# Optimization experiments

Measured on AMD Instinct MI355X. Metric: run time of the kernel, lower is better.

Reference implementation:

```python
import jax, jax.numpy as jnp
from jax import lax
import numpy as np

DN = ('NCWXYZ', 'OIWXYZ', 'NCWXYZ')  # 4 spatial dims W,X,Y,Z

def _conv4d(x, w, b):
    # x: [B, Cin, S, S, S, S]; w: [Cout, Cin, k, k, k, k]; valid padding, stride 1
    y = lax.conv_general_dilated(x, w, window_strides=(1, 1, 1, 1),
                                 padding='VALID', dimension_numbers=DN)
    return y + b[None, :, None, None, None, None]

def setup_inputs() -> dict:
    key = jax.random.key(0)
    ks = jax.random.split(key, 16)
    def rn(k, shape, fan_in):
        return jax.random.normal(k, shape, dtype=jnp.float32) * (2.0 / fan_in) ** 0.5
    B = 256
    x = jax.random.normal(ks[0], (B, 1, 18, 18, 18, 18), dtype=jnp.float32)
    w1 = rn(ks[1], (3, 1, 4, 4, 4, 4), 1 * 4**4); b1 = jnp.zeros((3,), jnp.float32)
    w2 = rn(ks[2], (3, 3, 4, 4, 4, 4), 3 * 4**4); b2 = jnp.zeros((3,), jnp.float32)
    w3 = rn(ks[3], (4, 3, 4, 4, 4, 4), 3 * 4**4); b3 = jnp.zeros((4,), jnp.float32)
    w4 = rn(ks[4], (5, 4, 4, 4, 4, 4), 4 * 4**4); b4 = jnp.zeros((5,), jnp.float32)
    w5 = rn(ks[5], (5, 5, 3, 3, 3, 3), 5 * 3**4); b5 = jnp.zeros((5,), jnp.float32)
    dw1 = rn(ks[6], (33, 1280), 1280); db1 = jnp.zeros((33,), jnp.float32)
    dw2 = rn(ks[7], (2, 33), 33); db2 = jnp.zeros((2,), jnp.float32)
    return {'x': x, 'w1': w1, 'b1': b1, 'w2': w2, 'b2': b2, 'w3': w3, 'b3': b3,
            'w4': w4, 'b4': b4, 'w5': w5, 'b5': b5,
            'dw1': dw1, 'db1': db1, 'dw2': dw2, 'db2': db2}

def reference(x, w1, b1, w2, b2, w3, b3, w4, b4, w5, b5, dw1, db1, dw2, db2):
    h = jax.nn.relu(_conv4d(x, w1, b1))   # [B,3,15,15,15,15]
    h = jax.nn.relu(_conv4d(h, w2, b2))   # [B,3,12,12,12,12]
    h = jax.nn.relu(_conv4d(h, w3, b3))   # [B,4,9,9,9,9]
    h = jax.nn.relu(_conv4d(h, w4, b4))   # [B,5,6,6,6,6]
    h = jax.nn.relu(_conv4d(h, w5, b5))   # [B,5,4,4,4,4]
    h = h.reshape(h.shape[0], -1)         # [B,1280]
    # Dropout treated as identity (eval-mode reference)
    h = jax.nn.relu(h @ dw1.T + db1)      # [B,33]
    return jax.nn.softmax(h @ dw2.T + db2, axis=1)  # [B,2]
```

## Files before the change

kernel.cpp:

```cpp
#include <hip/hip_runtime.h>
#include <hip/hip_bf16.h>
#include <math.h>


#define BATCH 256
typedef _Float16 half_t;
typedef _Float16 h2_t  __attribute__((ext_vector_type(2)));
typedef short    bf16x8 __attribute__((ext_vector_type(8)));
typedef float    f32x4 __attribute__((ext_vector_type(4)));
typedef unsigned int   uint32;
typedef unsigned short ushort16;

__device__ __forceinline__ float dot2f(uint32 a, uint32 b, float c) {
    return __builtin_amdgcn_fdot2(__builtin_bit_cast(h2_t, a),
                                  __builtin_bit_cast(h2_t, b), c, false);
}

__device__ __forceinline__ ushort16 f2bf(float f) {
    const uint32 u = __builtin_bit_cast(uint32, f);
    return (ushort16)((u + 0x7FFFu + ((u >> 16) & 1u)) >> 16);
}

__global__ void cvt_x_pad(const float* __restrict__ x,
                          ushort16* __restrict__ xp) {
    constexpr int CH  = 972;
    constexpr int NSL = BATCH * 18;
    const int c = blockIdx.x * blockDim.x + threadIdx.x;
    if (c >= NSL * CH) return;
    const int s   = c / CH;
    const int j   = c - s * CH;
    const int r   = j / 3;
    const int g   = j - 3 * r;
    const float* src = x + ((size_t)s * 324 + r) * 18 + 8 * g;
    uint32 w[4];
    if (g < 2) {
        #pragma unroll
        for (int q = 0; q < 4; ++q) {
            const float2 v = ((const float2*)src)[q];
            w[q] = (uint32)f2bf(v.x) | ((uint32)f2bf(v.y) << 16);
        }
    } else {
        const float2 v = *(const float2*)src;
        w[0] = (uint32)f2bf(v.x) | ((uint32)f2bf(v.y) << 16);
        w[1] = w[2] = w[3] = 0;
    }
    ((uint4*)xp)[c] = (uint4){w[0], w[1], w[2], w[3]};
}

template <int CIN, int COUT, int ISZ, int OSZ, int ZPK, int KS>
__device__ void pack_mfma_one(const float* __restrict__ w,
                              ushort16* __restrict__ Bq, int gtid, int gstride) {
    constexpr int TOT = 4 * KS * COUT * 512;
    for (int t = gtid; t < TOT; t += gstride) {
        const int h  = t & 7;
        const int l  = (t >> 3) & 63;
        const int f  = t >> 9;
        const int nt = f % COUT;
        const int ks = (f / COUT) % KS;
        const int kw = f / (COUT * KS);
        const int k  = ks * 32 + (l >> 4) * 8 + h;
        const int combo = k / ZPK;
        const int iz = k - combo * ZPK;
        const int ci = combo >> 4;
        const int kx = (combo >> 2) & 3;
        const int ky = combo & 3;
        const int oz = l & 15;
        const int kz = iz - oz;
        ushort16 v = 0;
        if (oz < OSZ && kz >= 0 && kz < 4 && iz < ISZ)
            v = f2bf(w[((((nt * CIN + ci) * 4 + kw) * 4 + kx) * 4 + ky) * 4 + kz]);
        Bq[t] = v;
    }
}

__global__ void pack_weights_mfma(const float* __restrict__ w1,
                                  const float* __restrict__ w2,
                                  const float* __restrict__ w3,
                                  ushort16* __restrict__ Bq1,
                                  ushort16* __restrict__ Bq2,
                                  ushort16* __restrict__ Bq3) {
    const int gtid = blockIdx.x * blockDim.x + threadIdx.x;
    const int gs   = gridDim.x * blockDim.x;
    pack_mfma_one<1, 3, 18, 15, 24, 12>(w1, Bq1, gtid, gs);
    pack_mfma_one<3, 3, 15, 12, 16, 24>(w2, Bq2, gtid, gs);
    pack_mfma_one<3, 4, 12,  9, 16, 24>(w3, Bq3, gtid, gs);
}

template <int CIN, int COUT, int ISZ, int OSZ, int ZPK, int KS,
          int MT_TOT, int NT, int IN_MODE, bool OUTF16>
__global__ __launch_bounds__(NT)
void conv4d_mfma(const void* __restrict__ in_v,
                 const ushort16* __restrict__ Bq,
                 const float* __restrict__ bias,
                 ushort16* __restrict__ out) {
    constexpr int K   = 4;
    constexpr int R2  = ISZ * ISZ;
    constexpr int NW  = NT / 64;
    constexpr int MT_PER = (MT_TOT + NW - 1) / NW;
    constexpr int SLAB = (CIN * R2 + 24) * ZPK;
    static_assert(CIN * 16 * ZPK == KS * 32, "K-dim bookkeeping");
    static_assert(ZPK % 8 == 0, "8-slice must not straddle combos");

    __shared__ ushort16 slab[SLAB];

    const int tid = threadIdx.x;
    const int l   = tid & 63;
    const int wv  = tid >> 6;
    const int b   = blockIdx.x / OSZ;
    const int ow  = blockIdx.x % OSZ;
    const int lg  = l >> 4;

    for (int t = tid; t < SLAB; t += NT) slab[t] = 0;

    int mbase[MT_PER];
    #pragma unroll
    for (int i = 0; i < MT_PER; ++i) {
        const int mt = wv + NW * i;
        const int m  = (mt < MT_TOT) ? (mt * 16 + (l & 15)) : 0;
        mbase[i] = (m / OSZ) * ISZ + (m % OSZ);
    }

    f32x4 acc[MT_PER][COUT];
    #pragma unroll
    for (int i = 0; i < MT_PER; ++i)
        #pragma unroll
        for (int nt = 0; nt < COUT; ++nt)
            acc[i][nt] = (f32x4){0.f, 0.f, 0.f, 0.f};

    for (int kw = 0; kw < K; ++kw) {
        __syncthreads();
        const int iw = ow + kw;
        if constexpr (IN_MODE == 0) {
            const float* g = (const float*)in_v +
                ((size_t)b * ISZ + iw) * (size_t)(R2 * ISZ);
            for (int t = tid; t < (R2 * ISZ) / 2; t += NT) {
                const float2 v = ((const float2*)g)[t];
                const int e = 2 * t;
                const int r = e / ISZ, z = e % ISZ;
                const uint32 pv = (uint32)f2bf(v.x) | ((uint32)f2bf(v.y) << 16);
                *(uint32*)&slab[r * ZPK + z] = pv;
            }
        } else {
            constexpr int CPR = ZPK / 8;
            constexpr int NCH = CIN * R2 * CPR;
            const ushort16* inp = (const ushort16*)in_v;
            for (int t = tid; t < NCH; t += NT) {
                const int ci  = t / (R2 * CPR);
                const int rem = t % (R2 * CPR);
                const uint4* g = (const uint4*)(inp +
                    ((size_t)(b * CIN + ci) * ISZ + iw) * (size_t)(R2 * ZPK));
                const uint4 v = g[rem];
                *(uint4*)&slab[(ci * R2) * ZPK + rem * 8] = v;
            }
        }
        __syncthreads();

        #pragma unroll 2
        for (int ks = 0; ks < KS; ++ks) {
            bf16x8 bq[COUT];
            const ushort16* bp = Bq + (size_t)((kw * KS + ks) * COUT) * 512 + l * 8;
            #pragma unroll
            for (int nt = 0; nt < COUT; ++nt)
                bq[nt] = *(const bf16x8*)(bp + nt * 512);
            const int k8    = ks * 32 + lg * 8;
            const int combo = k8 / ZPK;
            const int iz0   = k8 - combo * ZPK;
            const int ci    = combo >> 4;
            const int kx    = (combo >> 2) & 3;
            const int ky    = combo & 3;
            const int roff  = ci * R2 + kx * ISZ + ky;
            #pragma unroll
            for (int i = 0; i < MT_PER; ++i) {
                if (wv + NW * i < MT_TOT) {
                    const bf16x8 a =
                        *(const bf16x8*)&slab[(mbase[i] + roff) * ZPK + iz0];
                    #pragma unroll
                    for (int nt = 0; nt < COUT; ++nt)
                        acc[i][nt] = __builtin_amdgcn_mfma_f32_16x16x32_bf16(
                            a, bq[nt], acc[i][nt], 0, 0, 0);
                }
            }
        }
    }

    const int oz = l & 15;
    #pragma unroll
    for (int i = 0; i < MT_PER; ++i) {
        const int mt = wv + NW * i;
        if (mt < MT_TOT) {
            #pragma unroll
            for (int nt = 0; nt < COUT; ++nt) {
                const float bv = bias[nt];
                #pragma unroll
                for (int r = 0; r < 4; ++r) {
                    const int m = mt * 16 + (l >> 4) * 4 + r;
                    if (m < OSZ * OSZ) {
                        const int ox = m / OSZ, oy = m % OSZ;
                        const float vv = fmaxf(acc[i][nt][r] + bv, 0.f);
                        ushort16 bits;
                        if constexpr (OUTF16) {
                            const half_t hv = (half_t)vv;
                            bits = __builtin_bit_cast(ushort16, hv);
                        } else {
                            bits = f2bf(vv);
                        }
                        out[(((((size_t)b * COUT + nt) * OSZ + ow) * OSZ + ox)
                             * OSZ + oy) * 16 + oz] = bits;
                    }
                }
            }
        }
    }
}

template <int CIN, int COUT, int K, int ISZ, int OSZ,
          int IPG, int OPG, int ZP, int NT, bool INF32>
__global__ __launch_bounds__(NT)
void conv4d_relu_f16(const void* __restrict__ in_v,
                     const float* __restrict__ w,
                     const float* __restrict__ bias,
                     half_t* __restrict__ out) {
    constexpr int KP  = 4;
    constexpr int R2  = ISZ * ISZ;
    constexpr int WTOT = CIN * K * K * K * COUT * KP;
    constexpr int LINES = COUT * OSZ * OSZ;
    constexpr int NIT = (LINES + NT - 1) / NT;
    constexpr int RL  = OSZ + KP - 1;
    constexpr int RQ  = (RL + 7) / 8;
    constexpr int NW  = RQ * 4;
    constexpr int NODD = (OSZ + 2) / 2;

    static_assert(8 * RQ <= ZP, "row read overruns z-pad");
    static_assert(NODD + 1 <= NW, "perm source word out of range");

    __shared__ half_t sw[WTOT];
    __shared__ half_t slab[CIN * R2 * ZP];

    const int tid = threadIdx.x;
    const int b   = blockIdx.x / OSZ;
    const int ow  = blockIdx.x % OSZ;

    for (int t = tid; t < WTOT; t += NT) {
        const int kz = t % KP; int c = t / KP;
        const int co = c % COUT; c /= COUT;
        const int ky = c % K; c /= K;
        const int kx = c % K; c /= K;
        const int kw = c % K; const int ci = c / K;
        const float v = (kz < K)
            ? w[((((co * CIN + ci) * K + kw) * K + kx) * K + ky) * K + kz]
            : 0.0f;
        sw[t] = (half_t)v;
    }

    float acc[NIT][OSZ];
    #pragma unroll
    for (int it = 0; it < NIT; ++it) {
        const int line = tid + it * NT;
        const float bv = (line < LINES) ? bias[line % COUT] : 0.0f;
        #pragma unroll
        for (int oz = 0; oz < OSZ; ++oz) acc[it][oz] = bv;
    }

    for (int kw = 0; kw < K; ++kw) {
        __syncthreads();
        const int iw = ow + kw;
        if constexpr (INF32) {
            const float* g = (const float*)in_v + ((size_t)b * ISZ + iw) * (size_t)(R2 * ISZ);
            for (int t = tid; t < R2 * ISZ; t += NT) {
                const int r = t / ISZ, z = t % ISZ;
                slab[r * ZP + z] = (half_t)g[t];
            }
        } else {
            constexpr int CPR = IPG / 8;
            constexpr int NCH = CIN * R2 * CPR;
            const half_t* inp = (const half_t*)in_v;
            for (int t = tid; t < NCH; t += NT) {
                const int ci  = t / (R2 * CPR);
                const int rem = t % (R2 * CPR);
                const int r = rem / CPR, c = rem % CPR;
                const uint4* g = (const uint4*)(inp +
                    ((size_t)(b * CIN + ci) * ISZ + iw) * (size_t)(R2 * IPG));
                const uint4 v = g[rem];
                *(uint4*)&slab[(ci * R2 + r) * ZP + 8 * c] = v;
            }
        }
        __syncthreads();

        #pragma unroll
        for (int it = 0; it < NIT; ++it) {
            const int line = tid + it * NT;
            if (line >= LINES) continue;
            const int co = line % COUT;
            const int xy = line / COUT;
            const int ox = xy / OSZ;
            const int oy = xy % OSZ;
            #pragma unroll 1
            for (int ci = 0; ci < CIN; ++ci) {
                #pragma unroll 1
                for (int kx = 0; kx < K; ++kx) {
                    #pragma unroll
                    for (int ky = 0; ky < K; ++ky) {
                        const half_t* rp = &slab[((ci * ISZ + ox + kx) * ISZ + oy + ky) * ZP];
                        uint32 wd[NW];
                        #pragma unroll
                        for (int q = 0; q < RQ; ++q) {
                            const uint4 v = ((const uint4*)rp)[q];
                            wd[4*q+0] = v.x; wd[4*q+1] = v.y;
                            wd[4*q+2] = v.z; wd[4*q+3] = v.w;
                        }
                        uint32 od[NODD];
                        #pragma unroll
                        for (int i = 0; i < NODD; ++i)
                            od[i] = __builtin_amdgcn_perm(wd[i + 1], wd[i], 0x05040302u);
                        const int wb = ((((ci * K + kw) * K + kx) * K + ky) * COUT + co) * KP;
                        const uint2 wv = *(const uint2*)&sw[wb];
                        #pragma unroll
                        for (int oz = 0; oz < OSZ; ++oz) {
                            const int s1 = oz + 2;
                            const uint32 p0 = (oz & 1) ? od[oz >> 1] : wd[oz >> 1];
                            const uint32 p1 = (s1 & 1) ? od[s1 >> 1] : wd[s1 >> 1];
                            acc[it][oz] = dot2f(p0, wv.x, dot2f(p1, wv.y, acc[it][oz]));
                        }
                    }
                }
            }
        }
    }

    #pragma unroll
    for (int it = 0; it < NIT; ++it) {
        const int line = tid + it * NT;
        if (line >= LINES) continue;
        const int co = line % COUT;
        const int xy = line / COUT;
        const int ox = xy / OSZ;
        const int oy = xy % OSZ;
        half_t* op = out + (((((size_t)b * COUT + co) * OSZ + ow) * OSZ + ox) * OSZ + oy) * OPG;
        #pragma unroll
        for (int p = 0; p < OSZ / 2; ++p) {
            h2_t pv = { (half_t)fmaxf(acc[it][2*p],     0.0f),
                        (half_t)fmaxf(acc[it][2*p + 1], 0.0f) };
            ((uint32*)op)[p] = __builtin_bit_cast(uint32, pv);
        }
        if constexpr (OSZ & 1)
            op[OSZ - 1] = (half_t)fmaxf(acc[it][OSZ - 1], 0.0f);
    }
}

__global__ void dense1_relu_f16(const half_t* __restrict__ h,
                                const float* __restrict__ w,
                                const float* __restrict__ bias,
                                float* __restrict__ out) {
    int idx = blockIdx.x * blockDim.x + threadIdx.x;
    if (idx >= BATCH * 33) return;
    const int j = idx % 33;
    const int i = idx / 33;
    const half_t* hr = h + (size_t)i * 1280;
    const float*  wr = w + (size_t)j * 1280;
    float a0 = bias[j], a1 = 0.f, a2 = 0.f, a3 = 0.f;
    for (int k = 0; k < 1280; k += 4) {
        a0 = fmaf((float)hr[k + 0], wr[k + 0], a0);
        a1 = fmaf((float)hr[k + 1], wr[k + 1], a1);
        a2 = fmaf((float)hr[k + 2], wr[k + 2], a2);
        a3 = fmaf((float)hr[k + 3], wr[k + 3], a3);
    }
    out[idx] = fmaxf((a0 + a1) + (a2 + a3), 0.0f);
}

__global__ void dense2_softmax(const float* __restrict__ h,
                               const float* __restrict__ w,
                               const float* __restrict__ bias,
                               float* __restrict__ out) {
    int i = blockIdx.x * blockDim.x + threadIdx.x;
    if (i >= BATCH) return;
    const float* hr = h + (size_t)i * 33;
    float a0 = bias[0], a1 = bias[1];
    for (int k = 0; k < 33; ++k) {
        a0 = fmaf(hr[k], w[k], a0);
        a1 = fmaf(hr[k], w[33 + k], a1);
    }
    const float m = fmaxf(a0, a1);
    const float e0 = expf(a0 - m);
    const float e1 = expf(a1 - m);
    const float s = e0 + e1;
    out[i * 2 + 0] = e0 / s;
    out[i * 2 + 1] = e1 / s;
}

extern "C" void kernel_launch(void* const* d_in, const int* in_sizes, int n_in,
                              void* d_out, int out_size, void* d_ws, size_t ws_size,
                              hipStream_t stream) {
    const float* x   = (const float*)d_in[0];
    const float* w1  = (const float*)d_in[1];
    const float* b1  = (const float*)d_in[2];
    const float* w2  = (const float*)d_in[3];
    const float* b2  = (const float*)d_in[4];
    const float* w3  = (const float*)d_in[5];
    const float* b3  = (const float*)d_in[6];
    const float* w4  = (const float*)d_in[7];
    const float* b4  = (const float*)d_in[8];
    const float* w5  = (const float*)d_in[9];
    const float* b5  = (const float*)d_in[10];
    const float* dw1 = (const float*)d_in[11];
    const float* db1 = (const float*)d_in[12];
    const float* dw2 = (const float*)d_in[13];
    const float* db2 = (const float*)d_in[14];

    ushort16* wsA = (ushort16*)d_ws;
    ushort16* wsB = wsA + 42000000;

    ushort16* h1 = wsA;
    ushort16* xp = wsB;
    ushort16* h2 = wsB;
    ushort16* h3 = wsA;
    half_t*   h4 = (half_t*)wsB;
    half_t*   h5 = (half_t*)wsA;
    float*    h6 = (float*)(wsB + 8000000);
    ushort16* Bq1 = wsA + 41500000;
    ushort16* Bq2 = wsA + 41600000;
    ushort16* Bq3 = wsA + 41760000;
    float* outp = (float*)d_out;

    const bool big_ws = ws_size >= (size_t)155663616ull;

    hipLaunchKernelGGL(pack_weights_mfma, dim3(64), dim3(256), 0, stream,
                       w1, w2, w3, Bq1, Bq2, Bq3);

    if (big_ws) {
        constexpr int NCH = BATCH * 18 * 972;
        hipLaunchKernelGGL(cvt_x_pad, dim3((NCH + 255) / 256), dim3(256),
                           0, stream, x, xp);
        hipLaunchKernelGGL((conv4d_mfma<1, 3, 18, 15, 24, 12, 15, 256, 2, false>),
                           dim3(BATCH * 15), dim3(256), 0, stream, xp, Bq1, b1, h1);
    } else {
        hipLaunchKernelGGL((conv4d_mfma<1, 3, 18, 15, 24, 12, 15, 256, 0, false>),
                           dim3(BATCH * 15), dim3(256), 0, stream, x, Bq1, b1, h1);
    }
    hipLaunchKernelGGL((conv4d_mfma<3, 3, 15, 12, 16, 24, 9, 256, 2, false>),
                       dim3(BATCH * 12), dim3(256), 0, stream, h1, Bq2, b2, h2);
    hipLaunchKernelGGL((conv4d_mfma<3, 4, 12, 9, 16, 24, 6, 256, 2, true>),
                       dim3(BATCH * 9), dim3(256), 0, stream, h2, Bq3, b3, h3);
    hipLaunchKernelGGL((conv4d_relu_f16<4, 5, 4, 9, 6, 16, 8, 24, 192, false>),
                       dim3(BATCH * 6), dim3(192), 0, stream, h3, w4, b4, h4);
    hipLaunchKernelGGL((conv4d_relu_f16<5, 5, 3, 6, 4, 8, 4, 8, 128, false>),
                       dim3(BATCH * 4), dim3(128), 0, stream, h4, w5, b5, h5);
    {
        dim3 grid((BATCH * 33 + 255) / 256);
        hipLaunchKernelGGL(dense1_relu_f16, grid, dim3(256), 0, stream, h5, dw1, db1, h6);
    }
    {
        hipLaunchKernelGGL(dense2_softmax, dim3(1), dim3(256), 0, stream,
                           h6, dw2, db2, outp);
    }
}
```

Baseline: 759.4 us.

## Move conv layer 4 onto bf16 MFMA path and pad LDS slab stride

Layer 4 now runs on the MFMA bf16 implicit-GEMM kernel with a new weight-packing kernel, replacing the scalar f16 dot-product kernel. Layer 3 output switches from f16 to bf16 to feed it. The conv kernel gains separate LDS row stride (ZS), input z-stride (IPZ) and output z-stride (OZS) parameters, so slab rows are padded to 24 elements, likely to reduce LDS bank conflicts. Risks include precision change and the extra pack launch.

```diff
diff --git a/kernel.cpp b/kernel.cpp
--- a/kernel.cpp
+++ b/kernel.cpp
@@ -86,8 +86,15 @@
     pack_mfma_one<3, 4, 12,  9, 16, 24>(w3, Bq3, gtid, gs);
 }
 
+__global__ void pack_weights_mfma4(const float* __restrict__ w4,
+                                   ushort16* __restrict__ Bq4) {
+    const int gtid = blockIdx.x * blockDim.x + threadIdx.x;
+    const int gs   = gridDim.x * blockDim.x;
+    pack_mfma_one<4, 5, 9, 6, 16, 32>(w4, Bq4, gtid, gs);
+}
+
 template <int CIN, int COUT, int ISZ, int OSZ, int ZPK, int KS,
-          int MT_TOT, int NT, int IN_MODE, bool OUTF16>
+          int MT_TOT, int NT, int IN_MODE, bool OUTF16, int ZS, int IPZ, int OZS>
 __global__ __launch_bounds__(NT)
 void conv4d_mfma(const void* __restrict__ in_v,
                  const ushort16* __restrict__ Bq,
@@ -97,9 +104,10 @@
     constexpr int R2  = ISZ * ISZ;
     constexpr int NW  = NT / 64;
     constexpr int MT_PER = (MT_TOT + NW - 1) / NW;
-    constexpr int SLAB = (CIN * R2 + 24) * ZPK;
+    constexpr int SLAB = (CIN * R2 + 24) * ZS;
     static_assert(CIN * 16 * ZPK == KS * 32, "K-dim bookkeeping");
     static_assert(ZPK % 8 == 0, "8-slice must not straddle combos");
+    static_assert(ZS >= ZPK && IPZ >= ZPK, "strides must cover logical K rows");
 
     __shared__ ushort16 slab[SLAB];
 
@@ -138,19 +146,26 @@
                 const int e = 2 * t;
                 const int r = e / ISZ, z = e % ISZ;
                 const uint32 pv = (uint32)f2bf(v.x) | ((uint32)f2bf(v.y) << 16);
-                *(uint32*)&slab[r * ZPK + z] = pv;
+                *(uint32*)&slab[r * ZS + z] = pv;
             }
         } else {
-            constexpr int CPR = ZPK / 8;
+            constexpr int CPR = IPZ / 8;
             constexpr int NCH = CIN * R2 * CPR;
             const ushort16* inp = (const ushort16*)in_v;
             for (int t = tid; t < NCH; t += NT) {
                 const int ci  = t / (R2 * CPR);
                 const int rem = t % (R2 * CPR);
                 const uint4* g = (const uint4*)(inp +
-                    ((size_t)(b * CIN + ci) * ISZ + iw) * (size_t)(R2 * ZPK));
+                    ((size_t)(b * CIN + ci) * ISZ + iw) * (size_t)(R2 * IPZ));
                 const uint4 v = g[rem];
-                *(uint4*)&slab[(ci * R2) * ZPK + rem * 8] = v;
+                int dst;
+                if constexpr (IPZ == ZS) {
+                    dst = (ci * R2) * ZS + rem * 8;
+                } else {
+                    const int r = rem / CPR, c = rem % CPR;
+                    dst = (ci * R2 + r) * ZS + c * 8;
+                }
+                *(uint4*)&slab[dst] = v;
             }
         }
         __syncthreads();
@@ -173,7 +188,7 @@
             for (int i = 0; i < MT_PER; ++i) {
                 if (wv + NW * i < MT_TOT) {
                     const bf16x8 a =
-                        *(const bf16x8*)&slab[(mbase[i] + roff) * ZPK + iz0];
+                        *(const bf16x8*)&slab[(mbase[i] + roff) * ZS + iz0];
                     #pragma unroll
                     for (int nt = 0; nt < COUT; ++nt)
                         acc[i][nt] = __builtin_amdgcn_mfma_f32_16x16x32_bf16(
@@ -187,7 +202,7 @@
     #pragma unroll
     for (int i = 0; i < MT_PER; ++i) {
         const int mt = wv + NW * i;
-        if (mt < MT_TOT) {
+        if (mt < MT_TOT && oz < OZS) {
             #pragma unroll
             for (int nt = 0; nt < COUT; ++nt) {
                 const float bv = bias[nt];
@@ -205,7 +220,7 @@
                             bits = f2bf(vv);
                         }
                         out[(((((size_t)b * COUT + nt) * OSZ + ow) * OSZ + ox)
-                             * OSZ + oy) * 16 + oz] = bits;
+                             * OSZ + oy) * OZS + oz] = bits;
                     }
                 }
             }
@@ -419,6 +434,7 @@
     ushort16* Bq1 = wsA + 41500000;
     ushort16* Bq2 = wsA + 41600000;
     ushort16* Bq3 = wsA + 41760000;
+    ushort16* Bq4 = wsA + 30000000;
     float* outp = (float*)d_out;
 
     const bool big_ws = ws_size >= (size_t)155663616ull;
@@ -430,18 +446,21 @@
         constexpr int NCH = BATCH * 18 * 972;
         hipLaunchKernelGGL(cvt_x_pad, dim3((NCH + 255) / 256), dim3(256),
                            0, stream, x, xp);
-        hipLaunchKernelGGL((conv4d_mfma<1, 3, 18, 15, 24, 12, 15, 256, 2, false>),
+        hipLaunchKernelGGL((conv4d_mfma<1, 3, 18, 15, 24, 12, 15, 256, 2, false, 24, 24, 16>),
                            dim3(BATCH * 15), dim3(256), 0, stream, xp, Bq1, b1, h1);
     } else {
-        hipLaunchKernelGGL((conv4d_mfma<1, 3, 18, 15, 24, 12, 15, 256, 0, false>),
+        hipLaunchKernelGGL((conv4d_mfma<1, 3, 18, 15, 24, 12, 15, 256, 0, false, 24, 24, 16>),
                            dim3(BATCH * 15), dim3(256), 0, stream, x, Bq1, b1, h1);
     }
-    hipLaunchKernelGGL((conv4d_mfma<3, 3, 15, 12, 16, 24, 9, 256, 2, false>),
+    hipLaunchKernelGGL((conv4d_mfma<3, 3, 15, 12, 16, 24, 9, 256, 2, false, 24, 16, 16>),
                        dim3(BATCH * 12), dim3(256), 0, stream, h1, Bq2, b2, h2);
-    hipLaunchKernelGGL((conv4d_mfma<3, 4, 12, 9, 16, 24, 6, 256, 2, true>),
+    hipLaunchKernelGGL(pack_weights_mfma4, dim3(64), dim3(256), 0, stream,
+                       w4, Bq4);
+    hipLaunchKernelGGL((conv4d_mfma<3, 4, 12, 9, 16, 24, 6, 256, 2, false, 24, 16, 16>),
                        dim3(BATCH * 9), dim3(256), 0, stream, h2, Bq3, b3, h3);
-    hipLaunchKernelGGL((conv4d_relu_f16<4, 5, 4, 9, 6, 16, 8, 24, 192, false>),
-                       dim3(BATCH * 6), dim3(192), 0, stream, h3, w4, b4, h4);
+    hipLaunchKernelGGL((conv4d_mfma<4, 5, 9, 6, 16, 32, 3, 192, 2, true, 24, 16, 8>),
+                       dim3(BATCH * 6), dim3(192), 0, stream, h3, Bq4, b4,
+                       (ushort16*)h4);
     hipLaunchKernelGGL((conv4d_relu_f16<5, 5, 3, 6, 4, 8, 4, 8, 128, false>),
                        dim3(BATCH * 4), dim3(128), 0, stream, h4, w5, b5, h5);
     {
```

Result: slower. 827.4 us (+9.0%).
